# Optimization experiments

Measured on AMD Instinct MI355X. Metric: run time of the kernel, lower is better.

Reference implementation:

```python
import jax, jax.numpy as jnp
import numpy as np

DG, UF, Z, FD = 32, 4, 16, 16      # decoder grid, upsample factor, z bins, feat dim
H = W = DG * UF                     # 128 BEV resolution
S = 128                             # depth samples per ray
MLP_H = 32
X_MIN, X_MAX = -51.2, 51.2
Y_MIN, Y_MAX = -51.2, 51.2
Z_MIN, Z_MAX = -5.0, 3.0
D_MIN, D_MAX = 1.0, 50.0


def setup_inputs() -> dict:
    key = jax.random.key(0)
    ks = jax.random.split(key, 8)
    B, R, D = 2, 8192, 512
    out_dim = UF * UF * Z * FD
    s1 = 1.0 / np.sqrt(D); s2 = 1.0 / np.sqrt(FD); s3 = 1.0 / np.sqrt(MLP_H)
    return {
        'decoder_output': jax.random.normal(ks[0], (B, DG * DG, D), jnp.float32),
        'ray_origins': jax.random.normal(ks[1], (B, R, 3), jnp.float32),
        'ray_directions': jax.random.normal(ks[2], (B, R, 3), jnp.float32),
        'ln_g': jnp.ones((D,), jnp.float32),
        'ln_b': jnp.zeros((D,), jnp.float32),
        'W1': jax.random.uniform(ks[3], (D, out_dim), jnp.float32, -s1, s1),
        'b1': jnp.zeros((out_dim,), jnp.float32),
        'W2': jax.random.uniform(ks[4], (FD, MLP_H), jnp.float32, -s2, s2),
        'b2': jnp.zeros((MLP_H,), jnp.float32),
        'W3': jax.random.uniform(ks[5], (MLP_H, 1), jnp.float32, -s3, s3),
        'b3': jnp.zeros((1,), jnp.float32),
    }


def _build_nfg(dec, ln_g, ln_b, W1, b1):
    B = dec.shape[0]
    mu = dec.mean(-1, keepdims=True)
    var = dec.var(-1, keepdims=True)  # biased, matches torch LayerNorm
    x = (dec - mu) / jnp.sqrt(var + 1e-5) * ln_g + ln_b
    x = x @ W1 + b1
    x = x.reshape(B, DG, DG, UF, UF, Z, FD).transpose(0, 1, 3, 2, 4, 5, 6)
    x = x.reshape(B, H, W, Z, FD)
    return x.transpose(0, 4, 3, 1, 2)  # (B, F, Z, H, W)


def _trilinear_one(nfg_b, cw, ch, cd):
    # nfg_b: (F, Z, H, W); cw/ch/cd: (P,) in [-1,1] indexing W/H/Z resp.
    # align_corners=True mapping, zeros padding (mask OOB corners).
    fw = (cw + 1.0) * 0.5 * (W - 1)
    fh = (ch + 1.0) * 0.5 * (H - 1)
    fd = (cd + 1.0) * 0.5 * (Z - 1)
    w0 = jnp.floor(fw); h0 = jnp.floor(fh); d0 = jnp.floor(fd)
    tw = fw - w0; th = fh - h0; td = fd - d0
    out = jnp.zeros((nfg_b.shape[0], cw.shape[0]), nfg_b.dtype)
    for dd in (0, 1):
        for hh in (0, 1):
            for ww in (0, 1):
                di = d0 + dd; hi = h0 + hh; wi = w0 + ww
                wt = ((td if dd else 1.0 - td) * (th if hh else 1.0 - th)
                      * (tw if ww else 1.0 - tw))
                valid = ((di >= 0) & (di <= Z - 1) & (hi >= 0) & (hi <= H - 1)
                         & (wi >= 0) & (wi <= W - 1))
                dic = jnp.clip(di, 0, Z - 1).astype(jnp.int32)
                hic = jnp.clip(hi, 0, H - 1).astype(jnp.int32)
                wic = jnp.clip(wi, 0, W - 1).astype(jnp.int32)
                out = out + nfg_b[:, dic, hic, wic] * (wt * valid)
    return out  # (F, P)


def reference(decoder_output, ray_origins, ray_directions,
              ln_g, ln_b, W1, b1, W2, b2, W3, b3):
    nfg = _build_nfg(decoder_output, ln_g, ln_b, W1, b1)  # (B,F,Z,H,W)
    B, R, _ = ray_origins.shape
    t = jnp.linspace(0.0, 1.0, S, dtype=jnp.float32)
    depths = D_MIN + (D_MAX - D_MIN) * t                       # (S,)
    pts = ray_origins[:, :, None, :] + ray_directions[:, :, None, :] * depths[None, None, :, None]
    xn = 2.0 * (pts[..., 0] - X_MIN) / (X_MAX - X_MIN) - 1.0
    yn = 2.0 * (pts[..., 1] - Y_MIN) / (Y_MAX - Y_MIN) - 1.0
    zn = 2.0 * (pts[..., 2] - Z_MIN) / (Z_MAX - Z_MIN) - 1.0
    # torch grid_sample grid last dim = (x,y,z) -> (W,H,D); grid was stacked [y,x,z]
    cw = yn.reshape(B, -1); ch = xn.reshape(B, -1); cd = zn.reshape(B, -1)
    feats = jax.vmap(_trilinear_one)(nfg, cw, ch, cd)          # (B, F, R*S)
    feats = feats.transpose(0, 2, 1).reshape(B, R, S, FD)
    h = jax.nn.relu(feats @ W2 + b2)
    alpha = jax.nn.sigmoid((h @ W3 + b3)[..., 0])              # (B, R, S)
    oma = 1.0 - alpha + 1e-10
    trans = jnp.cumprod(
        jnp.concatenate([jnp.ones((B, R, 1), alpha.dtype), oma[..., :-1]], -1), -1)
    weights = alpha * trans
    pred_depths = (weights * depths[None, None, :]).sum(-1)    # (B, R)
    return pred_depths, weights, nfg
```

## Files before the change

kernel.cpp:

```cpp
#include <hip/hip_runtime.h>
#include <math.h>

#define DG   32
#define UF   4
#define ZB   16
#define FD   16
#define HH   128
#define WWID 128
#define SNUM 128
#define BATCH 2
#define RAYS  8192
#define NTOK  2048
#define DINP  512
#define ODIM  4096
#define MLPH  32

#define OUT_PRED_OFF 0
#define OUT_W_OFF    (BATCH*RAYS)
#define OUT_NFG_OFF  (OUT_W_OFF + BATCH*RAYS*SNUM)

typedef _Float16 half8 __attribute__((ext_vector_type(8)));
typedef _Float16 half4 __attribute__((ext_vector_type(4)));
typedef _Float16 h2 __attribute__((ext_vector_type(2)));
typedef float f32x4 __attribute__((ext_vector_type(4)));

#define GLDS16(gp, lp) \
    __builtin_amdgcn_global_load_lds((const __attribute__((address_space(1))) void*)(gp), \
                                     (__attribute__((address_space(3))) void*)(lp), 16, 0, 0)

__global__ __launch_bounds__(256) void prep_kernel(const float* __restrict__ dec,
                                                   const float* __restrict__ lng,
                                                   const float* __restrict__ lnb,
                                                   const float* __restrict__ W2,
                                                   const float* __restrict__ b2,
                                                   const float* __restrict__ W3,
                                                   const float* __restrict__ W1,
                                                   _Float16* __restrict__ Af,
                                                   _Float16* __restrict__ W1T,
                                                   _Float16* __restrict__ W2f,
                                                   float* __restrict__ b2f,
                                                   float* __restrict__ w3f) {
    int tid = threadIdx.x;
    if (blockIdx.x < NTOK) {
        int t = blockIdx.x;
        const float2* row = reinterpret_cast<const float2*>(dec + (size_t)t * DINP);
        float2 v = row[tid];

        __shared__ float red[4];
        __shared__ float stat[2];

        float s = v.x + v.y;
        #pragma unroll
        for (int o = 32; o > 0; o >>= 1) s += __shfl_down(s, o);
        if ((tid & 63) == 0) red[tid >> 6] = s;
        __syncthreads();
        if (tid == 0) stat[0] = (red[0] + red[1] + red[2] + red[3]) * (1.0f / DINP);
        __syncthreads();
        float mu = stat[0];

        float dx = v.x - mu, dy = v.y - mu;
        float q = dx * dx + dy * dy;
        #pragma unroll
        for (int o = 32; o > 0; o >>= 1) q += __shfl_down(q, o);
        if ((tid & 63) == 0) red[tid >> 6] = q;
        __syncthreads();
        if (tid == 0) {
            float var = (red[0] + red[1] + red[2] + red[3]) * (1.0f / DINP);
            stat[1] = 1.0f / sqrtf(var + 1e-5f);
        }
        __syncthreads();
        float rstd = stat[1];

        int c = 2 * tid;
        h2 o2;
        o2.x = (_Float16)(dx * rstd * lng[c]     + lnb[c]);
        o2.y = (_Float16)(dy * rstd * lng[c + 1] + lnb[c + 1]);
        *reinterpret_cast<h2*>(Af + (size_t)t * DINP + c) = o2;

        if (blockIdx.x == 0 && tid < 128) {
            int jt = tid >> 6, l = tid & 63;
            int sub = l & 15, g = l >> 4;
            #pragma unroll
            for (int e = 0; e < 4; ++e) {
                W2f[(jt * 64 + l) * 4 + e] = (_Float16)W2[(g * 4 + e) * MLPH + jt * 16 + sub];
                b2f[(jt * 64 + l) * 4 + e] = b2[jt * 16 + g * 4 + e];
                w3f[(jt * 64 + l) * 4 + e] = W3[jt * 16 + g * 4 + e];
            }
        }
    } else {
        __shared__ float st[64][65];
        int blk = blockIdx.x - NTOK;
        int c0 = (blk & 63) * 64;
        int k0 = (blk >> 6) * 64;
        {
            int r = tid >> 2, cq = (tid & 3) * 16;
            const float* src = W1 + (size_t)(k0 + r) * ODIM + c0 + cq;
            #pragma unroll
            for (int qq = 0; qq < 4; ++qq) {
                float4 v = *reinterpret_cast<const float4*>(src + qq * 4);
                st[r][cq + qq * 4 + 0] = v.x;
                st[r][cq + qq * 4 + 1] = v.y;
                st[r][cq + qq * 4 + 2] = v.z;
                st[r][cq + qq * 4 + 3] = v.w;
            }
        }
        __syncthreads();
        {
            int cc = tid >> 2, kq = (tid & 3) * 16;
            _Float16 tmp[16];
            #pragma unroll
            for (int i = 0; i < 16; ++i) tmp[i] = (_Float16)st[kq + i][cc];
            _Float16* dst = W1T + (size_t)(c0 + cc) * DINP + k0 + kq;
            *reinterpret_cast<half8*>(dst)     = *reinterpret_cast<half8*>(&tmp[0]);
            *reinterpret_cast<half8*>(dst + 8) = *reinterpret_cast<half8*>(&tmp[8]);
        }
    }
}

__global__ __launch_bounds__(256, 2) void gemm_mfma_kernel(
        const _Float16* __restrict__ Af, const _Float16* __restrict__ W1T,
        const float* __restrict__ bias, _Float16* __restrict__ gh) {
    __shared__ _Float16 As[128 * 32];
    __shared__ _Float16 Bs[128 * 32];

    int tid = threadIdx.x;
    int l = tid & 63, w = tid >> 6;
    int wr = w >> 1, wc = w & 1;
    int row0 = blockIdx.y * 128;
    int col0 = blockIdx.x * 128;

    const char* Ag0 = (const char*)Af + (size_t)(row0 + w * 32 + (l >> 2)) * (DINP * 2) + (l & 3) * 16;
    const char* Ag1 = Ag0 + 16 * (DINP * 2);
    const char* Bg0 = (const char*)W1T + (size_t)(col0 + w * 32 + (l >> 2)) * (DINP * 2) + (l & 3) * 16;
    const char* Bg1 = Bg0 + 16 * (DINP * 2);
    char* lA0 = (char*)As + w * 2048;
    char* lA1 = lA0 + 1024;
    char* lB0 = (char*)Bs + w * 2048;
    char* lB1 = lB0 + 1024;

    f32x4 acc[4][4] = {};

    for (int kk = 0; kk < DINP; kk += 32) {
        GLDS16(Ag0, lA0); GLDS16(Ag1, lA1);
        GLDS16(Bg0, lB0); GLDS16(Bg1, lB1);
        Ag0 += 64; Ag1 += 64; Bg0 += 64; Bg1 += 64;
        __syncthreads();

        half8 af[4], bf[4];
        #pragma unroll
        for (int m = 0; m < 4; ++m)
            af[m] = *reinterpret_cast<const half8*>(As + (wr * 64 + m * 16 + (l & 15)) * 32 + (l >> 4) * 8);
        #pragma unroll
        for (int n = 0; n < 4; ++n)
            bf[n] = *reinterpret_cast<const half8*>(Bs + (wc * 64 + n * 16 + (l & 15)) * 32 + (l >> 4) * 8);
        #pragma unroll
        for (int m = 0; m < 4; ++m)
            #pragma unroll
            for (int n = 0; n < 4; ++n)
                acc[m][n] = __builtin_amdgcn_mfma_f32_16x16x32_f16(af[m], bf[n], acc[m][n], 0, 0, 0);
        __syncthreads();
    }

    #pragma unroll
    for (int n = 0; n < 4; ++n) {
        int c = col0 + wc * 64 + n * 16 + (l & 15);
        float bv = bias[c];
        int f = c & 15, z = (c >> 4) & 15, v = (c >> 8) & 3, u = (c >> 10) & 3;
        #pragma unroll
        for (int m = 0; m < 4; ++m) {
            int rbase = row0 + wr * 64 + m * 16 + ((l >> 4) << 2);
            #pragma unroll
            for (int j = 0; j < 4; ++j) {
                int t = rbase + j;
                int bb = t >> 10;
                int g = t & 1023;
                int i = g >> 5, j2 = g & 31;
                int h = i * 4 + u, wq = j2 * 4 + v;
                size_t gaddr = ((((size_t)(bb * ZB + z) * HH + h) * WWID + wq) << 4) + f;
                gh[gaddr] = (_Float16)(acc[m][n][j] + bv);
            }
        }
    }
}

__global__ __launch_bounds__(256) void tp_kernel(const _Float16* __restrict__ gh,
                                                 float* __restrict__ nfg) {
    int blk = blockIdx.x;
    int bb = blk >> 11, z = (blk >> 7) & 15, h = blk & 127;
    __shared__ float sl[128 * 17];
    int tid = threadIdx.x;
    const uint4* src = reinterpret_cast<const uint4*>(gh + (size_t)blk * 2048);
    uint4 v = src[tid];
    int wv = tid >> 1, fb = (tid & 1) * 8;
    h2 p0 = __builtin_bit_cast(h2, v.x);
    h2 p1 = __builtin_bit_cast(h2, v.y);
    h2 p2 = __builtin_bit_cast(h2, v.z);
    h2 p3 = __builtin_bit_cast(h2, v.w);
    float* sr = &sl[wv * 17 + fb];
    sr[0] = (float)p0.x; sr[1] = (float)p0.y;
    sr[2] = (float)p1.x; sr[3] = (float)p1.y;
    sr[4] = (float)p2.x; sr[5] = (float)p2.y;
    sr[6] = (float)p3.x; sr[7] = (float)p3.y;
    __syncthreads();
    int f = tid >> 4, w0 = (tid & 15) * 8;
    float* dst = nfg + (((size_t)(bb * FD + f) * ZB + z) * (HH * WWID)) + h * WWID + w0;
    float4 o0, o1;
    o0.x = sl[(w0 + 0) * 17 + f]; o0.y = sl[(w0 + 1) * 17 + f];
    o0.z = sl[(w0 + 2) * 17 + f]; o0.w = sl[(w0 + 3) * 17 + f];
    o1.x = sl[(w0 + 4) * 17 + f]; o1.y = sl[(w0 + 5) * 17 + f];
    o1.z = sl[(w0 + 6) * 17 + f]; o1.w = sl[(w0 + 7) * 17 + f];
    *reinterpret_cast<float4*>(dst) = o0;
    *reinterpret_cast<float4*>(dst + 4) = o1;
}

__device__ __forceinline__ void gather_feat(const _Float16* __restrict__ gb,
                                            float px, float py, float pz,
                                            h2* __restrict__ a) {
    float fw = (py * (1.0f / 51.2f) + 1.0f) * 63.5f;
    float fh = (px * (1.0f / 51.2f) + 1.0f) * 63.5f;
    float fd = (pz + 5.0f) * (0.25f * 7.5f);
    float w0f = floorf(fw), h0f = floorf(fh), d0f = floorf(fd);
    float tw = fw - w0f, th = fh - h0f, td = fd - d0f;
    int w0 = (int)w0f, h0 = (int)h0f, d0 = (int)d0f;

    float aw0 = (w0 >= 0 && w0 <= WWID - 1) ? (1.0f - tw) : 0.0f;
    float aw1 = (w0 + 1 >= 0 && w0 + 1 <= WWID - 1) ? tw : 0.0f;
    float ah0 = (h0 >= 0 && h0 <= HH - 1) ? (1.0f - th) : 0.0f;
    float ah1 = (h0 + 1 >= 0 && h0 + 1 <= HH - 1) ? th : 0.0f;
    float ad0 = (d0 >= 0 && d0 <= ZB - 1) ? (1.0f - td) : 0.0f;
    float ad1 = (d0 + 1 >= 0 && d0 + 1 <= ZB - 1) ? td : 0.0f;

    if ((ad0 + ad1) * (ah0 + ah1) * (aw0 + aw1) <= 0.0f) return;

    int h0c = min(max(h0, 0), HH - 1),   h1c = min(max(h0 + 1, 0), HH - 1);
    int d0c = min(max(d0, 0), ZB - 1),   d1c = min(max(d0 + 1, 0), ZB - 1);
    int wb = min(max(w0, 0), WWID - 2);
    float ws0 = (wb == w0) ? aw0 : ((wb == w0 + 1) ? aw1 : 0.0f);
    float ws1 = (wb == w0) ? aw1 : ((wb == w0 - 1) ? aw0 : 0.0f);

    int od0 = d0c * (HH * WWID * FD), od1 = d1c * (HH * WWID * FD);
    int oh0 = h0c * (WWID * FD),      oh1 = h1c * (WWID * FD);
    int ow  = wb * FD;

#define CPAIR(OFF, WDH) do { \
        const uint4* cp_ = reinterpret_cast<const uint4*>(gb + (OFF)); \
        uint4 A_ = cp_[0], B_ = cp_[1], C_ = cp_[2], D_ = cp_[3]; \
        _Float16 u0_ = (_Float16)((WDH) * ws0); \
        _Float16 u1_ = (_Float16)((WDH) * ws1); \
        h2 W0_ = {u0_, u0_}; h2 W1_ = {u1_, u1_}; \
        a[0] += __builtin_bit_cast(h2, A_.x) * W0_; \
        a[1] += __builtin_bit_cast(h2, A_.y) * W0_; \
        a[2] += __builtin_bit_cast(h2, A_.z) * W0_; \
        a[3] += __builtin_bit_cast(h2, A_.w) * W0_; \
        a[4] += __builtin_bit_cast(h2, B_.x) * W0_; \
        a[5] += __builtin_bit_cast(h2, B_.y) * W0_; \
        a[6] += __builtin_bit_cast(h2, B_.z) * W0_; \
        a[7] += __builtin_bit_cast(h2, B_.w) * W0_; \
        a[0] += __builtin_bit_cast(h2, C_.x) * W1_; \
        a[1] += __builtin_bit_cast(h2, C_.y) * W1_; \
        a[2] += __builtin_bit_cast(h2, C_.z) * W1_; \
        a[3] += __builtin_bit_cast(h2, C_.w) * W1_; \
        a[4] += __builtin_bit_cast(h2, D_.x) * W1_; \
        a[5] += __builtin_bit_cast(h2, D_.y) * W1_; \
        a[6] += __builtin_bit_cast(h2, D_.z) * W1_; \
        a[7] += __builtin_bit_cast(h2, D_.w) * W1_; \
    } while (0)

    CPAIR(od0 + oh0 + ow, ad0 * ah0);
    CPAIR(od0 + oh1 + ow, ad0 * ah1);
    CPAIR(od1 + oh0 + ow, ad1 * ah0);
    CPAIR(od1 + oh1 + ow, ad1 * ah1);
#undef CPAIR
}

#define SF 24
__global__ __launch_bounds__(256) void ray_fused_kernel(
        const float* __restrict__ orig, const float* __restrict__ dirs,
        const _Float16* __restrict__ gh,
        const _Float16* __restrict__ W2f, const float* __restrict__ b2f,
        const float* __restrict__ w3f, const float* __restrict__ b3,
        float* __restrict__ pred_out, float* __restrict__ w_out) {
    int tid = threadIdx.x;
    int lane = tid & 63, wvid = tid >> 6;
    int ray = blockIdx.x * 4 + wvid;
    int bb = ray >> 13;

    __shared__ _Float16 featLDS[4 * 64 * SF];
    _Float16* FL = &featLDS[wvid * 64 * SF];

    const float* o3 = orig + (size_t)ray * 3;
    const float* d3 = dirs + (size_t)ray * 3;
    float ox = o3[0], oy = o3[1], oz = o3[2];
    float dx = d3[0], dy = d3[1], dz = d3[2];

    const _Float16* gb = gh + (size_t)bb * (ZB * HH * WWID * FD);

    float t0 = 1.0f + 49.0f * ((float)lane * (1.0f / 127.0f));
    float t1 = 1.0f + 49.0f * ((float)(lane + 64) * (1.0f / 127.0f));

    h2 acc0[8] = {}, acc1[8] = {};
    gather_feat(gb, ox + dx * t0, oy + dy * t0, oz + dz * t0, acc0);
    gather_feat(gb, ox + dx * t1, oy + dy * t1, oz + dz * t1, acc1);

    half4 Af0 = *reinterpret_cast<const half4*>(W2f + lane * 4);
    half4 Af1 = *reinterpret_cast<const half4*>(W2f + (64 + lane) * 4);
    f32x4 b20 = *reinterpret_cast<const f32x4*>(b2f + lane * 4);
    f32x4 b21 = *reinterpret_cast<const f32x4*>(b2f + (64 + lane) * 4);
    f32x4 w30 = *reinterpret_cast<const f32x4*>(w3f + lane * 4);
    f32x4 w31 = *reinterpret_cast<const f32x4*>(w3f + (64 + lane) * 4);
    float b3v = b3[0];

    float at[8];

    {
        uint4 p0, p1;
        p0.x = __builtin_bit_cast(unsigned int, acc0[0]);
        p0.y = __builtin_bit_cast(unsigned int, acc0[1]);
        p0.z = __builtin_bit_cast(unsigned int, acc0[2]);
        p0.w = __builtin_bit_cast(unsigned int, acc0[3]);
        p1.x = __builtin_bit_cast(unsigned int, acc0[4]);
        p1.y = __builtin_bit_cast(unsigned int, acc0[5]);
        p1.z = __builtin_bit_cast(unsigned int, acc0[6]);
        p1.w = __builtin_bit_cast(unsigned int, acc0[7]);
        *reinterpret_cast<uint4*>(FL + lane * SF)     = p0;
        *reinterpret_cast<uint4*>(FL + lane * SF + 8) = p1;
        #pragma unroll
        for (int tt = 0; tt < 4; ++tt) {
            half4 bfrag = *reinterpret_cast<const half4*>(
                FL + (tt * 16 + (lane & 15)) * SF + (lane >> 4) * 4);
            f32x4 c0 = __builtin_amdgcn_mfma_f32_16x16x16f16(Af0, bfrag, b20, 0, 0, 0);
            f32x4 c1 = __builtin_amdgcn_mfma_f32_16x16x16f16(Af1, bfrag, b21, 0, 0, 0);
            float p = 0.0f;
            #pragma unroll
            for (int r = 0; r < 4; ++r) {
                p = fmaf(fmaxf(c0[r], 0.0f), w30[r], p);
                p = fmaf(fmaxf(c1[r], 0.0f), w31[r], p);
            }
            p += __shfl_xor(p, 16);
            p += __shfl_xor(p, 32);
            at[tt] = p;
        }
    }
    {
        uint4 q0, q1;
        q0.x = __builtin_bit_cast(unsigned int, acc1[0]);
        q0.y = __builtin_bit_cast(unsigned int, acc1[1]);
        q0.z = __builtin_bit_cast(unsigned int, acc1[2]);
        q0.w = __builtin_bit_cast(unsigned int, acc1[3]);
        q1.x = __builtin_bit_cast(unsigned int, acc1[4]);
        q1.y = __builtin_bit_cast(unsigned int, acc1[5]);
        q1.z = __builtin_bit_cast(unsigned int, acc1[6]);
        q1.w = __builtin_bit_cast(unsigned int, acc1[7]);
        *reinterpret_cast<uint4*>(FL + lane * SF)     = q0;
        *reinterpret_cast<uint4*>(FL + lane * SF + 8) = q1;
        #pragma unroll
        for (int tt = 0; tt < 4; ++tt) {
            half4 bfrag = *reinterpret_cast<const half4*>(
                FL + (tt * 16 + (lane & 15)) * SF + (lane >> 4) * 4);
            f32x4 c0 = __builtin_amdgcn_mfma_f32_16x16x16f16(Af0, bfrag, b20, 0, 0, 0);
            f32x4 c1 = __builtin_amdgcn_mfma_f32_16x16x16f16(Af1, bfrag, b21, 0, 0, 0);
            float p = 0.0f;
            #pragma unroll
            for (int r = 0; r < 4; ++r) {
                p = fmaf(fmaxf(c0[r], 0.0f), w30[r], p);
                p = fmaf(fmaxf(c1[r], 0.0f), w31[r], p);
            }
            p += __shfl_xor(p, 16);
            p += __shfl_xor(p, 32);
            at[tt + 4] = p;
        }
    }

    int g2 = lane >> 4;
    float aS0 = at[0];
    aS0 = (g2 == 1) ? at[1] : aS0;
    aS0 = (g2 == 2) ? at[2] : aS0;
    aS0 = (g2 == 3) ? at[3] : aS0;
    float aS1 = at[4];
    aS1 = (g2 == 1) ? at[5] : aS1;
    aS1 = (g2 == 2) ? at[6] : aS1;
    aS1 = (g2 == 3) ? at[7] : aS1;
    aS0 += b3v; aS1 += b3v;

    float alpha0 = 1.0f / (1.0f + __expf(-aS0));
    float alpha1 = 1.0f / (1.0f + __expf(-aS1));
    float oma0 = 1.0f - alpha0 + 1e-10f;
    float oma1 = 1.0f - alpha1 + 1e-10f;

    float P = oma0;
    #pragma unroll
    for (int off = 1; off < 64; off <<= 1) {
        float u = __shfl_up(P, off);
        if (lane >= off) P *= u;
    }
    float T64 = __shfl(P, 63);
    float Q = oma1;
    #pragma unroll
    for (int off = 1; off < 64; off <<= 1) {
        float u = __shfl_up(Q, off);
        if (lane >= off) Q *= u;
    }
    float e0 = __shfl_up(P, 1);
    if (lane == 0) e0 = 1.0f;
    float e1 = __shfl_up(Q, 1);
    e1 = (lane == 0) ? T64 : e1 * T64;

    float w0 = alpha0 * e0;
    float w1 = alpha1 * e1;
    w_out[(size_t)ray * SNUM + lane] = w0;
    w_out[(size_t)ray * SNUM + 64 + lane] = w1;

    float pv = w0 * t0 + w1 * t1;
    #pragma unroll
    for (int o = 32; o > 0; o >>= 1) pv += __shfl_xor(pv, o);
    if (lane == 0) pred_out[ray] = pv;
}

extern "C" void kernel_launch(void* const* d_in, const int* in_sizes, int n_in,
                              void* d_out, int out_size, void* d_ws, size_t ws_size,
                              hipStream_t stream) {
    const float* dec = (const float*)d_in[0];
    const float* ro  = (const float*)d_in[1];
    const float* rd  = (const float*)d_in[2];
    const float* lng = (const float*)d_in[3];
    const float* lnb = (const float*)d_in[4];
    const float* W1  = (const float*)d_in[5];
    const float* b1  = (const float*)d_in[6];
    const float* W2  = (const float*)d_in[7];
    const float* b2  = (const float*)d_in[8];
    const float* W3  = (const float*)d_in[9];
    const float* b3  = (const float*)d_in[10];

    float* out = (float*)d_out;
    char*  wsb = (char*)d_ws;
    _Float16* Af  = (_Float16*)wsb;
    _Float16* W1T = (_Float16*)(wsb + (2u << 20));
    _Float16* gh  = (_Float16*)(wsb + (6u << 20));
    _Float16* W2f = (_Float16*)(wsb + (23u << 20));
    float*    b2f = (float*)(wsb + (23u << 20) + 4096);
    float*    w3f = (float*)(wsb + (23u << 20) + 8192);

    prep_kernel<<<NTOK + (ODIM / 64) * (DINP / 64), 256, 0, stream>>>(
        dec, lng, lnb, W2, b2, W3, W1, Af, W1T, W2f, b2f, w3f);

    dim3 gg(ODIM / 128, NTOK / 128);
    gemm_mfma_kernel<<<gg, 256, 0, stream>>>(Af, W1T, b1, gh);

    ray_fused_kernel<<<BATCH * RAYS / 4, 256, 0, stream>>>(ro, rd, gh, W2f, b2f, w3f, b3,
                                                           out + OUT_PRED_OFF, out + OUT_W_OFF);

    tp_kernel<<<BATCH * ZB * HH, 256, 0, stream>>>(gh, out + OUT_NFG_OFF);
}
```

Measured before the change: 63.57 us.

## Cooperative lane-shared trilinear gather with software-pipelined loads

Restructures the trilinear gather so each sample's four corner pairs are loaded by four cooperating lanes, using shuffles to broadcast offsets and weights. Each lane loads one 16-byte chunk per corner instead of 64 bytes, and a shuffle-xor reduction combines the two w-sides. Loads for the next group of 16 samples are issued before the current group is consumed, double-buffering global loads against the FMA work. This aims to improve coalescing and memory-level parallelism and to cut per-lane register pressure, at the cost of extra shuffles and more serialized rounds.

```diff
diff --git a/kernel.cpp b/kernel.cpp
--- a/kernel.cpp
+++ b/kernel.cpp
@@ -213,67 +213,71 @@
     *reinterpret_cast<float4*>(dst + 4) = o1;
 }
 
-__device__ __forceinline__ void gather_feat(const _Float16* __restrict__ gb,
-                                            float px, float py, float pz,
-                                            h2* __restrict__ a) {
-    float fw = (py * (1.0f / 51.2f) + 1.0f) * 63.5f;
-    float fh = (px * (1.0f / 51.2f) + 1.0f) * 63.5f;
-    float fd = (pz + 5.0f) * (0.25f * 7.5f);
-    float w0f = floorf(fw), h0f = floorf(fh), d0f = floorf(fd);
-    float tw = fw - w0f, th = fh - h0f, td = fd - d0f;
-    int w0 = (int)w0f, h0 = (int)h0f, d0 = (int)d0f;
-
-    float aw0 = (w0 >= 0 && w0 <= WWID - 1) ? (1.0f - tw) : 0.0f;
-    float aw1 = (w0 + 1 >= 0 && w0 + 1 <= WWID - 1) ? tw : 0.0f;
-    float ah0 = (h0 >= 0 && h0 <= HH - 1) ? (1.0f - th) : 0.0f;
-    float ah1 = (h0 + 1 >= 0 && h0 + 1 <= HH - 1) ? th : 0.0f;
-    float ad0 = (d0 >= 0 && d0 <= ZB - 1) ? (1.0f - td) : 0.0f;
-    float ad1 = (d0 + 1 >= 0 && d0 + 1 <= ZB - 1) ? td : 0.0f;
-
-    if ((ad0 + ad1) * (ah0 + ah1) * (aw0 + aw1) <= 0.0f) return;
-
-    int h0c = min(max(h0, 0), HH - 1),   h1c = min(max(h0 + 1, 0), HH - 1);
-    int d0c = min(max(d0, 0), ZB - 1),   d1c = min(max(d0 + 1, 0), ZB - 1);
-    int wb = min(max(w0, 0), WWID - 2);
-    float ws0 = (wb == w0) ? aw0 : ((wb == w0 + 1) ? aw1 : 0.0f);
-    float ws1 = (wb == w0) ? aw1 : ((wb == w0 - 1) ? aw0 : 0.0f);
-
-    int od0 = d0c * (HH * WWID * FD), od1 = d1c * (HH * WWID * FD);
-    int oh0 = h0c * (WWID * FD),      oh1 = h1c * (WWID * FD);
-    int ow  = wb * FD;
-
-#define CPAIR(OFF, WDH) do { \
-        const uint4* cp_ = reinterpret_cast<const uint4*>(gb + (OFF)); \
-        uint4 A_ = cp_[0], B_ = cp_[1], C_ = cp_[2], D_ = cp_[3]; \
-        _Float16 u0_ = (_Float16)((WDH) * ws0); \
-        _Float16 u1_ = (_Float16)((WDH) * ws1); \
-        h2 W0_ = {u0_, u0_}; h2 W1_ = {u1_, u1_}; \
-        a[0] += __builtin_bit_cast(h2, A_.x) * W0_; \
-        a[1] += __builtin_bit_cast(h2, A_.y) * W0_; \
-        a[2] += __builtin_bit_cast(h2, A_.z) * W0_; \
-        a[3] += __builtin_bit_cast(h2, A_.w) * W0_; \
-        a[4] += __builtin_bit_cast(h2, B_.x) * W0_; \
-        a[5] += __builtin_bit_cast(h2, B_.y) * W0_; \
-        a[6] += __builtin_bit_cast(h2, B_.z) * W0_; \
-        a[7] += __builtin_bit_cast(h2, B_.w) * W0_; \
-        a[0] += __builtin_bit_cast(h2, C_.x) * W1_; \
-        a[1] += __builtin_bit_cast(h2, C_.y) * W1_; \
-        a[2] += __builtin_bit_cast(h2, C_.z) * W1_; \
-        a[3] += __builtin_bit_cast(h2, C_.w) * W1_; \
-        a[4] += __builtin_bit_cast(h2, D_.x) * W1_; \
-        a[5] += __builtin_bit_cast(h2, D_.y) * W1_; \
-        a[6] += __builtin_bit_cast(h2, D_.z) * W1_; \
-        a[7] += __builtin_bit_cast(h2, D_.w) * W1_; \
-    } while (0)
-
-    CPAIR(od0 + oh0 + ow, ad0 * ah0);
-    CPAIR(od0 + oh1 + ow, ad0 * ah1);
-    CPAIR(od1 + oh0 + ow, ad1 * ah0);
-    CPAIR(od1 + oh1 + ow, ad1 * ah1);
-#undef CPAIR
-}
-
 #define SF 24
+
+struct RayCtx {
+    int   off[2][4];
+    float wdh[2][4];
+    float ws[2][2];
+    int   lv[2];
+};
+
+template <int R>
+__device__ __forceinline__ void rissue(const _Float16* __restrict__ gb,
+                                       int sq, int cch, int side,
+                                       const RayCtx& C,
+                                       uint4 (&L)[4], float (&u)[4], int& lv) {
+    constexpr int st = (R < 4) ? 0 : 1;
+    const int srcl = ((R % 4) * 16) + sq;
+    int o[4]; float wd[4];
+    #pragma unroll
+    for (int p = 0; p < 4; ++p) {
+        o[p]  = __shfl(C.off[st][p], srcl);
+        wd[p] = __shfl(C.wdh[st][p], srcl);
+    }
+    float wsa = __shfl(C.ws[st][0], srcl);
+    float wsb = __shfl(C.ws[st][1], srcl);
+    float wss = side ? wsb : wsa;
+    lv = __shfl(C.lv[st], srcl);
+    #pragma unroll
+    for (int p = 0; p < 4; ++p) u[p] = wd[p] * wss;
+    if (lv) {
+        #pragma unroll
+        for (int p = 0; p < 4; ++p)
+            L[p] = *reinterpret_cast<const uint4*>(gb + o[p] + cch * 8);
+    }
+}
+
+__device__ __forceinline__ void rconsume(_Float16* __restrict__ FL,
+                                         int row, int cch, int side,
+                                         const uint4 (&L)[4], const float (&u)[4],
+                                         int lv) {
+    h2 a0 = {}, a1 = {}, a2 = {}, a3 = {};
+    if (lv) {
+        #pragma unroll
+        for (int p = 0; p < 4; ++p) {
+            _Float16 uh = (_Float16)u[p];
+            h2 U = {uh, uh};
+            a0 += __builtin_bit_cast(h2, L[p].x) * U;
+            a1 += __builtin_bit_cast(h2, L[p].y) * U;
+            a2 += __builtin_bit_cast(h2, L[p].z) * U;
+            a3 += __builtin_bit_cast(h2, L[p].w) * U;
+        }
+    }
+    a0 += __builtin_bit_cast(h2, __shfl_xor(__builtin_bit_cast(int, a0), 2));
+    a1 += __builtin_bit_cast(h2, __shfl_xor(__builtin_bit_cast(int, a1), 2));
+    a2 += __builtin_bit_cast(h2, __shfl_xor(__builtin_bit_cast(int, a2), 2));
+    a3 += __builtin_bit_cast(h2, __shfl_xor(__builtin_bit_cast(int, a3), 2));
+    if (side == 0) {
+        uint4 o;
+        o.x = __builtin_bit_cast(unsigned int, a0);
+        o.y = __builtin_bit_cast(unsigned int, a1);
+        o.z = __builtin_bit_cast(unsigned int, a2);
+        o.w = __builtin_bit_cast(unsigned int, a3);
+        *reinterpret_cast<uint4*>(FL + row * SF + (cch & 1) * 8) = o;
+    }
+}
+
 __global__ __launch_bounds__(256) void ray_fused_kernel(
         const float* __restrict__ orig, const float* __restrict__ dirs,
         const _Float16* __restrict__ gh,
@@ -292,15 +296,45 @@
     const float* d3 = dirs + (size_t)ray * 3;
     float ox = o3[0], oy = o3[1], oz = o3[2];
     float dx = d3[0], dy = d3[1], dz = d3[2];
-
     const _Float16* gb = gh + (size_t)bb * (ZB * HH * WWID * FD);
 
     float t0 = 1.0f + 49.0f * ((float)lane * (1.0f / 127.0f));
     float t1 = 1.0f + 49.0f * ((float)(lane + 64) * (1.0f / 127.0f));
 
-    h2 acc0[8] = {}, acc1[8] = {};
-    gather_feat(gb, ox + dx * t0, oy + dy * t0, oz + dz * t0, acc0);
-    gather_feat(gb, ox + dx * t1, oy + dy * t1, oz + dz * t1, acc1);
+    RayCtx C;
+    #pragma unroll
+    for (int ss = 0; ss < 2; ++ss) {
+        float t = ss ? t1 : t0;
+        float px = ox + dx * t, py = oy + dy * t, pz = oz + dz * t;
+        float fw = (py * (1.0f / 51.2f) + 1.0f) * 63.5f;
+        float fh = (px * (1.0f / 51.2f) + 1.0f) * 63.5f;
+        float fd = (pz + 5.0f) * (0.25f * 7.5f);
+        float w0f = floorf(fw), h0f = floorf(fh), d0f = floorf(fd);
+        float tw = fw - w0f, th = fh - h0f, td = fd - d0f;
+        int w0 = (int)w0f, h0 = (int)h0f, d0 = (int)d0f;
+        float aw0 = (w0 >= 0 && w0 <= WWID - 1) ? (1.0f - tw) : 0.0f;
+        float aw1 = (w0 + 1 >= 0 && w0 + 1 <= WWID - 1) ? tw : 0.0f;
+        float ah0 = (h0 >= 0 && h0 <= HH - 1) ? (1.0f - th) : 0.0f;
+        float ah1 = (h0 + 1 >= 0 && h0 + 1 <= HH - 1) ? th : 0.0f;
+        float ad0 = (d0 >= 0 && d0 <= ZB - 1) ? (1.0f - td) : 0.0f;
+        float ad1 = (d0 + 1 >= 0 && d0 + 1 <= ZB - 1) ? td : 0.0f;
+        C.lv[ss] = ((ad0 + ad1) * (ah0 + ah1) * (aw0 + aw1) > 0.0f) ? 1 : 0;
+        int h0c = min(max(h0, 0), HH - 1), h1c = min(max(h0 + 1, 0), HH - 1);
+        int d0c = min(max(d0, 0), ZB - 1), d1c = min(max(d0 + 1, 0), ZB - 1);
+        int wb = min(max(w0, 0), WWID - 2);
+        float ws0 = (wb == w0) ? aw0 : ((wb == w0 + 1) ? aw1 : 0.0f);
+        float ws1 = (wb == w0) ? aw1 : ((wb == w0 - 1) ? aw0 : 0.0f);
+        int od0 = d0c * (HH * WWID * FD), od1 = d1c * (HH * WWID * FD);
+        int oh0 = h0c * (WWID * FD), oh1 = h1c * (WWID * FD);
+        int ow = wb * FD;
+        C.off[ss][0] = od0 + oh0 + ow; C.off[ss][1] = od0 + oh1 + ow;
+        C.off[ss][2] = od1 + oh0 + ow; C.off[ss][3] = od1 + oh1 + ow;
+        C.wdh[ss][0] = ad0 * ah0; C.wdh[ss][1] = ad0 * ah1;
+        C.wdh[ss][2] = ad1 * ah0; C.wdh[ss][3] = ad1 * ah1;
+        C.ws[ss][0] = ws0; C.ws[ss][1] = ws1;
+    }
+
+    int sq = lane >> 2, cch = lane & 3, side = cch >> 1;
 
     half4 Af0 = *reinterpret_cast<const half4*>(W2f + lane * 4);
     half4 Af1 = *reinterpret_cast<const half4*>(W2f + (64 + lane) * 4);
@@ -310,65 +344,59 @@
     f32x4 w31 = *reinterpret_cast<const f32x4*>(w3f + (64 + lane) * 4);
     float b3v = b3[0];
 
+    uint4 L0[4], L1[4]; float u0[4], u1[4]; int lv0, lv1;
     float at[8];
 
-    {
-        uint4 p0, p1;
-        p0.x = __builtin_bit_cast(unsigned int, acc0[0]);
-        p0.y = __builtin_bit_cast(unsigned int, acc0[1]);
-        p0.z = __builtin_bit_cast(unsigned int, acc0[2]);
-        p0.w = __builtin_bit_cast(unsigned int, acc0[3]);
-        p1.x = __builtin_bit_cast(unsigned int, acc0[4]);
-        p1.y = __builtin_bit_cast(unsigned int, acc0[5]);
-        p1.z = __builtin_bit_cast(unsigned int, acc0[6]);
-        p1.w = __builtin_bit_cast(unsigned int, acc0[7]);
-        *reinterpret_cast<uint4*>(FL + lane * SF)     = p0;
-        *reinterpret_cast<uint4*>(FL + lane * SF + 8) = p1;
-        #pragma unroll
-        for (int tt = 0; tt < 4; ++tt) {
-            half4 bfrag = *reinterpret_cast<const half4*>(
-                FL + (tt * 16 + (lane & 15)) * SF + (lane >> 4) * 4);
-            f32x4 c0 = __builtin_amdgcn_mfma_f32_16x16x16f16(Af0, bfrag, b20, 0, 0, 0);
-            f32x4 c1 = __builtin_amdgcn_mfma_f32_16x16x16f16(Af1, bfrag, b21, 0, 0, 0);
-            float p = 0.0f;
-            #pragma unroll
-            for (int r = 0; r < 4; ++r) {
-                p = fmaf(fmaxf(c0[r], 0.0f), w30[r], p);
-                p = fmaf(fmaxf(c1[r], 0.0f), w31[r], p);
-            }
-            p += __shfl_xor(p, 16);
-            p += __shfl_xor(p, 32);
-            at[tt] = p;
-        }
-    }
-    {
-        uint4 q0, q1;
-        q0.x = __builtin_bit_cast(unsigned int, acc1[0]);
-        q0.y = __builtin_bit_cast(unsigned int, acc1[1]);
-        q0.z = __builtin_bit_cast(unsigned int, acc1[2]);
-        q0.w = __builtin_bit_cast(unsigned int, acc1[3]);
-        q1.x = __builtin_bit_cast(unsigned int, acc1[4]);
-        q1.y = __builtin_bit_cast(unsigned int, acc1[5]);
-        q1.z = __builtin_bit_cast(unsigned int, acc1[6]);
-        q1.w = __builtin_bit_cast(unsigned int, acc1[7]);
-        *reinterpret_cast<uint4*>(FL + lane * SF)     = q0;
-        *reinterpret_cast<uint4*>(FL + lane * SF + 8) = q1;
-        #pragma unroll
-        for (int tt = 0; tt < 4; ++tt) {
-            half4 bfrag = *reinterpret_cast<const half4*>(
-                FL + (tt * 16 + (lane & 15)) * SF + (lane >> 4) * 4);
-            f32x4 c0 = __builtin_amdgcn_mfma_f32_16x16x16f16(Af0, bfrag, b20, 0, 0, 0);
-            f32x4 c1 = __builtin_amdgcn_mfma_f32_16x16x16f16(Af1, bfrag, b21, 0, 0, 0);
-            float p = 0.0f;
-            #pragma unroll
-            for (int r = 0; r < 4; ++r) {
-                p = fmaf(fmaxf(c0[r], 0.0f), w30[r], p);
-                p = fmaf(fmaxf(c1[r], 0.0f), w31[r], p);
-            }
-            p += __shfl_xor(p, 16);
-            p += __shfl_xor(p, 32);
-            at[tt + 4] = p;
-        }
+    rissue<0>(gb, sq, cch, side, C, L0, u0, lv0);
+    rissue<1>(gb, sq, cch, side, C, L1, u1, lv1);
+    rconsume(FL, 0 * 16 + sq, cch, side, L0, u0, lv0);
+    rissue<2>(gb, sq, cch, side, C, L0, u0, lv0);
+    rconsume(FL, 1 * 16 + sq, cch, side, L1, u1, lv1);
+    rissue<3>(gb, sq, cch, side, C, L1, u1, lv1);
+    rconsume(FL, 2 * 16 + sq, cch, side, L0, u0, lv0);
+    rissue<4>(gb, sq, cch, side, C, L0, u0, lv0);
+    rconsume(FL, 3 * 16 + sq, cch, side, L1, u1, lv1);
+
+    #pragma unroll
+    for (int tt = 0; tt < 4; ++tt) {
+        half4 bfrag = *reinterpret_cast<const half4*>(
+            FL + (tt * 16 + (lane & 15)) * SF + (lane >> 4) * 4);
+        f32x4 c0 = __builtin_amdgcn_mfma_f32_16x16x16f16(Af0, bfrag, b20, 0, 0, 0);
+        f32x4 c1 = __builtin_amdgcn_mfma_f32_16x16x16f16(Af1, bfrag, b21, 0, 0, 0);
+        float p = 0.0f;
+        #pragma unroll
+        for (int r = 0; r < 4; ++r) {
+            p = fmaf(fmaxf(c0[r], 0.0f), w30[r], p);
+            p = fmaf(fmaxf(c1[r], 0.0f), w31[r], p);
+        }
+        p += __shfl_xor(p, 16);
+        p += __shfl_xor(p, 32);
+        at[tt] = p;
+    }
+
+    rissue<5>(gb, sq, cch, side, C, L1, u1, lv1);
+    rconsume(FL, 0 * 16 + sq, cch, side, L0, u0, lv0);
+    rissue<6>(gb, sq, cch, side, C, L0, u0, lv0);
+    rconsume(FL, 1 * 16 + sq, cch, side, L1, u1, lv1);
+    rissue<7>(gb, sq, cch, side, C, L1, u1, lv1);
+    rconsume(FL, 2 * 16 + sq, cch, side, L0, u0, lv0);
+    rconsume(FL, 3 * 16 + sq, cch, side, L1, u1, lv1);
+
+    #pragma unroll
+    for (int tt = 0; tt < 4; ++tt) {
+        half4 bfrag = *reinterpret_cast<const half4*>(
+            FL + (tt * 16 + (lane & 15)) * SF + (lane >> 4) * 4);
+        f32x4 c0 = __builtin_amdgcn_mfma_f32_16x16x16f16(Af0, bfrag, b20, 0, 0, 0);
+        f32x4 c1 = __builtin_amdgcn_mfma_f32_16x16x16f16(Af1, bfrag, b21, 0, 0, 0);
+        float p = 0.0f;
+        #pragma unroll
+        for (int r = 0; r < 4; ++r) {
+            p = fmaf(fmaxf(c0[r], 0.0f), w30[r], p);
+            p = fmaf(fmaxf(c1[r], 0.0f), w31[r], p);
+        }
+        p += __shfl_xor(p, 16);
+        p += __shfl_xor(p, 32);
+        at[tt + 4] = p;
     }
 
     int g2 = lane >> 4;
```

Measured after the change: 75.64 us. 1.19x slower.

## Split each ray across two wavefronts with LDS transmittance exchange

Applied to the files above, without the earlier changes.

Each ray's 128 samples are now handled by two wavefronts of 64 samples each, not one wavefront doing both halves serially. The grid doubles, and the first half's transmittance and partial depth sum are passed to the second half through shared memory after a block barrier. The aim is more parallelism and less per-thread register pressure for latency hiding in the gather-bound ray kernel. The cost is a __syncthreads per block and twice as many waves loading the same ray origin, direction and MLP weights.

```diff
diff --git a/kernel.cpp b/kernel.cpp
--- a/kernel.cpp
+++ b/kernel.cpp
@@ -282,25 +282,39 @@
         float* __restrict__ pred_out, float* __restrict__ w_out) {
     int tid = threadIdx.x;
     int lane = tid & 63, wvid = tid >> 6;
-    int ray = blockIdx.x * 4 + wvid;
+    int rloc = wvid >> 1, half = wvid & 1;
+    int ray = blockIdx.x * 2 + rloc;
     int bb = ray >> 13;
 
     __shared__ _Float16 featLDS[4 * 64 * SF];
+    __shared__ float xch[4];
     _Float16* FL = &featLDS[wvid * 64 * SF];
 
     const float* o3 = orig + (size_t)ray * 3;
     const float* d3 = dirs + (size_t)ray * 3;
     float ox = o3[0], oy = o3[1], oz = o3[2];
     float dx = d3[0], dy = d3[1], dz = d3[2];
-
     const _Float16* gb = gh + (size_t)bb * (ZB * HH * WWID * FD);
 
-    float t0 = 1.0f + 49.0f * ((float)lane * (1.0f / 127.0f));
-    float t1 = 1.0f + 49.0f * ((float)(lane + 64) * (1.0f / 127.0f));
-
-    h2 acc0[8] = {}, acc1[8] = {};
-    gather_feat(gb, ox + dx * t0, oy + dy * t0, oz + dz * t0, acc0);
-    gather_feat(gb, ox + dx * t1, oy + dy * t1, oz + dz * t1, acc1);
+    int s = half * 64 + lane;
+    float t = 1.0f + 49.0f * ((float)s * (1.0f / 127.0f));
+
+    h2 acc[8] = {};
+    gather_feat(gb, ox + dx * t, oy + dy * t, oz + dz * t, acc);
+
+    {
+        uint4 p0, p1;
+        p0.x = __builtin_bit_cast(unsigned int, acc[0]);
+        p0.y = __builtin_bit_cast(unsigned int, acc[1]);
+        p0.z = __builtin_bit_cast(unsigned int, acc[2]);
+        p0.w = __builtin_bit_cast(unsigned int, acc[3]);
+        p1.x = __builtin_bit_cast(unsigned int, acc[4]);
+        p1.y = __builtin_bit_cast(unsigned int, acc[5]);
+        p1.z = __builtin_bit_cast(unsigned int, acc[6]);
+        p1.w = __builtin_bit_cast(unsigned int, acc[7]);
+        *reinterpret_cast<uint4*>(FL + lane * SF)     = p0;
+        *reinterpret_cast<uint4*>(FL + lane * SF + 8) = p1;
+    }
 
     half4 Af0 = *reinterpret_cast<const half4*>(W2f + lane * 4);
     half4 Af1 = *reinterpret_cast<const half4*>(W2f + (64 + lane) * 4);
@@ -310,110 +324,62 @@
     f32x4 w31 = *reinterpret_cast<const f32x4*>(w3f + (64 + lane) * 4);
     float b3v = b3[0];
 
-    float at[8];
-
-    {
-        uint4 p0, p1;
-        p0.x = __builtin_bit_cast(unsigned int, acc0[0]);
-        p0.y = __builtin_bit_cast(unsigned int, acc0[1]);
-        p0.z = __builtin_bit_cast(unsigned int, acc0[2]);
-        p0.w = __builtin_bit_cast(unsigned int, acc0[3]);
-        p1.x = __builtin_bit_cast(unsigned int, acc0[4]);
-        p1.y = __builtin_bit_cast(unsigned int, acc0[5]);
-        p1.z = __builtin_bit_cast(unsigned int, acc0[6]);
-        p1.w = __builtin_bit_cast(unsigned int, acc0[7]);
-        *reinterpret_cast<uint4*>(FL + lane * SF)     = p0;
-        *reinterpret_cast<uint4*>(FL + lane * SF + 8) = p1;
-        #pragma unroll
-        for (int tt = 0; tt < 4; ++tt) {
-            half4 bfrag = *reinterpret_cast<const half4*>(
-                FL + (tt * 16 + (lane & 15)) * SF + (lane >> 4) * 4);
-            f32x4 c0 = __builtin_amdgcn_mfma_f32_16x16x16f16(Af0, bfrag, b20, 0, 0, 0);
-            f32x4 c1 = __builtin_amdgcn_mfma_f32_16x16x16f16(Af1, bfrag, b21, 0, 0, 0);
-            float p = 0.0f;
-            #pragma unroll
-            for (int r = 0; r < 4; ++r) {
-                p = fmaf(fmaxf(c0[r], 0.0f), w30[r], p);
-                p = fmaf(fmaxf(c1[r], 0.0f), w31[r], p);
-            }
-            p += __shfl_xor(p, 16);
-            p += __shfl_xor(p, 32);
-            at[tt] = p;
-        }
-    }
-    {
-        uint4 q0, q1;
-        q0.x = __builtin_bit_cast(unsigned int, acc1[0]);
-        q0.y = __builtin_bit_cast(unsigned int, acc1[1]);
-        q0.z = __builtin_bit_cast(unsigned int, acc1[2]);
-        q0.w = __builtin_bit_cast(unsigned int, acc1[3]);
-        q1.x = __builtin_bit_cast(unsigned int, acc1[4]);
-        q1.y = __builtin_bit_cast(unsigned int, acc1[5]);
-        q1.z = __builtin_bit_cast(unsigned int, acc1[6]);
-        q1.w = __builtin_bit_cast(unsigned int, acc1[7]);
-        *reinterpret_cast<uint4*>(FL + lane * SF)     = q0;
-        *reinterpret_cast<uint4*>(FL + lane * SF + 8) = q1;
-        #pragma unroll
-        for (int tt = 0; tt < 4; ++tt) {
-            half4 bfrag = *reinterpret_cast<const half4*>(
-                FL + (tt * 16 + (lane & 15)) * SF + (lane >> 4) * 4);
-            f32x4 c0 = __builtin_amdgcn_mfma_f32_16x16x16f16(Af0, bfrag, b20, 0, 0, 0);
-            f32x4 c1 = __builtin_amdgcn_mfma_f32_16x16x16f16(Af1, bfrag, b21, 0, 0, 0);
-            float p = 0.0f;
-            #pragma unroll
-            for (int r = 0; r < 4; ++r) {
-                p = fmaf(fmaxf(c0[r], 0.0f), w30[r], p);
-                p = fmaf(fmaxf(c1[r], 0.0f), w31[r], p);
-            }
-            p += __shfl_xor(p, 16);
-            p += __shfl_xor(p, 32);
-            at[tt + 4] = p;
-        }
-    }
-
+    float at[4];
+    #pragma unroll
+    for (int tt = 0; tt < 4; ++tt) {
+        half4 bfrag = *reinterpret_cast<const half4*>(
+            FL + (tt * 16 + (lane & 15)) * SF + (lane >> 4) * 4);
+        f32x4 c0 = __builtin_amdgcn_mfma_f32_16x16x16f16(Af0, bfrag, b20, 0, 0, 0);
+        f32x4 c1 = __builtin_amdgcn_mfma_f32_16x16x16f16(Af1, bfrag, b21, 0, 0, 0);
+        float p = 0.0f;
+        #pragma unroll
+        for (int r = 0; r < 4; ++r) {
+            p = fmaf(fmaxf(c0[r], 0.0f), w30[r], p);
+            p = fmaf(fmaxf(c1[r], 0.0f), w31[r], p);
+        }
+        p += __shfl_xor(p, 16);
+        p += __shfl_xor(p, 32);
+        at[tt] = p;
+    }
     int g2 = lane >> 4;
-    float aS0 = at[0];
-    aS0 = (g2 == 1) ? at[1] : aS0;
-    aS0 = (g2 == 2) ? at[2] : aS0;
-    aS0 = (g2 == 3) ? at[3] : aS0;
-    float aS1 = at[4];
-    aS1 = (g2 == 1) ? at[5] : aS1;
-    aS1 = (g2 == 2) ? at[6] : aS1;
-    aS1 = (g2 == 3) ? at[7] : aS1;
-    aS0 += b3v; aS1 += b3v;
-
-    float alpha0 = 1.0f / (1.0f + __expf(-aS0));
-    float alpha1 = 1.0f / (1.0f + __expf(-aS1));
-    float oma0 = 1.0f - alpha0 + 1e-10f;
-    float oma1 = 1.0f - alpha1 + 1e-10f;
-
-    float P = oma0;
+    float aS = at[0];
+    aS = (g2 == 1) ? at[1] : aS;
+    aS = (g2 == 2) ? at[2] : aS;
+    aS = (g2 == 3) ? at[3] : aS;
+    aS += b3v;
+
+    float alpha = 1.0f / (1.0f + __expf(-aS));
+    float oma = 1.0f - alpha + 1e-10f;
+
+    float P = oma;
     #pragma unroll
     for (int off = 1; off < 64; off <<= 1) {
         float u = __shfl_up(P, off);
         if (lane >= off) P *= u;
     }
-    float T64 = __shfl(P, 63);
-    float Q = oma1;
-    #pragma unroll
-    for (int off = 1; off < 64; off <<= 1) {
-        float u = __shfl_up(Q, off);
-        if (lane >= off) Q *= u;
-    }
-    float e0 = __shfl_up(P, 1);
-    if (lane == 0) e0 = 1.0f;
-    float e1 = __shfl_up(Q, 1);
-    e1 = (lane == 0) ? T64 : e1 * T64;
-
-    float w0 = alpha0 * e0;
-    float w1 = alpha1 * e1;
-    w_out[(size_t)ray * SNUM + lane] = w0;
-    w_out[(size_t)ray * SNUM + 64 + lane] = w1;
-
-    float pv = w0 * t0 + w1 * t1;
-    #pragma unroll
-    for (int o = 32; o > 0; o >>= 1) pv += __shfl_xor(pv, o);
-    if (lane == 0) pred_out[ray] = pv;
+    float T = __shfl(P, 63);
+    float e = __shfl_up(P, 1);
+    if (lane == 0) e = 1.0f;
+
+    if (half == 0) {
+        float wv = alpha * e;
+        w_out[(size_t)ray * SNUM + lane] = wv;
+        float pv = wv * t;
+        #pragma unroll
+        for (int o = 32; o > 0; o >>= 1) pv += __shfl_xor(pv, o);
+        if (lane == 0) { xch[rloc * 2] = T; xch[rloc * 2 + 1] = pv; }
+    }
+    __syncthreads();
+    if (half == 1) {
+        float T0 = xch[rloc * 2];
+        float es = (lane == 0) ? T0 : e * T0;
+        float wv = alpha * es;
+        w_out[(size_t)ray * SNUM + 64 + lane] = wv;
+        float pv = wv * t;
+        #pragma unroll
+        for (int o = 32; o > 0; o >>= 1) pv += __shfl_xor(pv, o);
+        if (lane == 0) pred_out[ray] = pv + xch[rloc * 2 + 1];
+    }
 }
 
 extern "C" void kernel_launch(void* const* d_in, const int* in_sizes, int n_in,
@@ -446,7 +412,7 @@
     dim3 gg(ODIM / 128, NTOK / 128);
     gemm_mfma_kernel<<<gg, 256, 0, stream>>>(Af, W1T, b1, gh);
 
-    ray_fused_kernel<<<BATCH * RAYS / 4, 256, 0, stream>>>(ro, rd, gh, W2f, b2f, w3f, b3,
+    ray_fused_kernel<<<BATCH * RAYS / 2, 256, 0, stream>>>(ro, rd, gh, W2f, b2f, w3f, b3,
                                                            out + OUT_PRED_OFF, out + OUT_W_OFF);
 
     tp_kernel<<<BATCH * ZB * HH, 256, 0, stream>>>(gh, out + OUT_NFG_OFF);
```

Result: slower. 70.26 us (+10.5%).
